# Optimization experiments

Measured on AMD Instinct MI355X. Metric: run time of the kernel, lower is better.

The kernel has to match this reference:

```python
import jax, jax.numpy as jnp
import numpy as np

B, S, D, H = 2, 2048, 1024, 16
DK = D // H


def setup_inputs() -> dict:
    key = jax.random.key(0)
    ks = jax.random.split(key, 12)
    scale = 1.0 / np.sqrt(D)
    inp = {
        "query": jax.random.normal(ks[0], (B, S, D), jnp.float32),
        "key": jax.random.normal(ks[1], (B, S, D), jnp.float32),
        "value": jax.random.normal(ks[2], (B, S, D), jnp.float32),
        "mask": jax.random.randint(ks[3], (B, 1, S, S), 0, 2, jnp.int32),
        "Wq": jax.random.normal(ks[4], (D, D), jnp.float32) * scale,
        "bq": jnp.zeros((D,), jnp.float32),
        "Wk": jax.random.normal(ks[5], (D, D), jnp.float32) * scale,
        "bk": jnp.zeros((D,), jnp.float32),
        "Wv": jax.random.normal(ks[6], (D, D), jnp.float32) * scale,
        "bv": jnp.zeros((D,), jnp.float32),
        "Wo": jax.random.normal(ks[7], (D, D), jnp.float32) * scale,
        "bo": jnp.zeros((D,), jnp.float32),
    }
    return inp


def reference(query, key, value, mask, Wq, bq, Wk, bk, Wv, bv, Wo, bo):
    # Linear projections (dropout is identity in eval mode)
    q = query @ Wq + bq          # (B,S,D)
    k = key @ Wk + bk
    v = value @ Wv + bv

    # split heads: (B,S,D) -> (B,H,S,DK)
    def split(x):
        return x.reshape(B, S, H, DK).transpose(0, 2, 1, 3)

    q, k, v = split(q), split(k), split(v)

    scores = jnp.einsum("bhqd,bhkd->bhqk", q, k) / jnp.sqrt(jnp.float32(DK))
    scores = jnp.where(mask == 0, jnp.float32(-1e9), scores)
    p_attn = jax.nn.softmax(scores, axis=-1)   # (B,H,S,S)

    att = jnp.einsum("bhqk,bhkd->bhqd", p_attn, v)  # (B,H,S,DK)
    merged = att.transpose(0, 2, 1, 3).reshape(B, S, D)
    return merged @ Wo + bo
```

## Files before the change

### kernel.cpp

```cpp
#include <hip/hip_runtime.h>
#include <hip/hip_bf16.h>
#include <cstdint>
#include <cstddef>


#define B_ 2
#define S_ 2048
#define D_ 1024
#define H_ 16
#define M_ 4096

typedef unsigned short u16;
typedef __attribute__((ext_vector_type(8))) short bf16x8;
typedef __attribute__((ext_vector_type(8))) unsigned short u16x8;
typedef __attribute__((ext_vector_type(4))) unsigned short u16x4;
typedef __attribute__((ext_vector_type(4))) unsigned int u32x4;
typedef __attribute__((ext_vector_type(4))) float f32x4;
typedef __attribute__((ext_vector_type(4))) int i32x4;

#define QSCALE 0.18033688011112042f

__device__ __forceinline__ u16 f2bf(float f) {
  __hip_bfloat16 h = __float2bfloat16(f);
  return *reinterpret_cast<u16*>(&h);
}

__device__ __forceinline__ unsigned cvtpk(float lo, float hi) {
  unsigned r;
  asm("v_cvt_pk_bf16_f32 %0, %1, %2" : "=v"(r) : "v"(lo), "v"(hi));
  return r;
}

__device__ __forceinline__ void gload_lds16(const void* g, void* l) {
  __builtin_amdgcn_global_load_lds((const __attribute__((address_space(1))) void*)g,
                                   (__attribute__((address_space(3))) void*)l, 16, 0, 0);
}

__global__ __launch_bounds__(256) void k_convert(const float* __restrict__ q, const float* __restrict__ k,
                                                 const float* __restrict__ v,
                                                 u16* __restrict__ xq, u16* __restrict__ xk, u16* __restrict__ xv) {
  int z = blockIdx.y;
  const float* src = (z == 0) ? q : (z == 1) ? k : v;
  u16* dst = (z == 0) ? xq : (z == 1) ? xk : xv;
  size_t i = ((size_t)blockIdx.x * 256 + threadIdx.x) * 8;
  f32x4 a = *(const f32x4*)(src + i);
  f32x4 b = *(const f32x4*)(src + i + 4);
  u16x8 o;
  o[0]=f2bf(a[0]); o[1]=f2bf(a[1]); o[2]=f2bf(a[2]); o[3]=f2bf(a[3]);
  o[4]=f2bf(b[0]); o[5]=f2bf(b[1]); o[6]=f2bf(b[2]); o[7]=f2bf(b[3]);
  *(u16x8*)(dst + i) = o;
}

__global__ __launch_bounds__(256) void k_transposeW(const float* __restrict__ w0, const float* __restrict__ w1,
                                                    const float* __restrict__ w2, const float* __restrict__ w3,
                                                    u16* __restrict__ t0, u16* __restrict__ t1,
                                                    u16* __restrict__ t2, u16* __restrict__ t3) {
  int z = blockIdx.z;
  const float* W = (z==0)?w0:(z==1)?w1:(z==2)?w2:w3;
  u16* Wt = (z==0)?t0:(z==1)?t1:(z==2)?t2:t3;
  __shared__ float tile[32][33];
  int tx = threadIdx.x & 31, ty = threadIdx.x >> 5;
  int bx = blockIdx.x * 32, by = blockIdx.y * 32;
  #pragma unroll
  for (int p = 0; p < 4; ++p)
    tile[ty + p*8][tx] = W[(size_t)(by + ty + p*8) * D_ + bx + tx];
  __syncthreads();
  #pragma unroll
  for (int p = 0; p < 4; ++p)
    Wt[(size_t)(bx + ty + p*8) * D_ + by + tx] = f2bf(tile[tx][ty + p*8]);
}

__global__ __launch_bounds__(256) void k_packmask(const int* __restrict__ mask, u16* __restrict__ out) {
  size_t t = (size_t)blockIdx.x * 256 + threadIdx.x;
  const int* p = mask + t * 64;
  unsigned wds0 = 0, wds1 = 0, wds2 = 0, wds3 = 0;
  #pragma unroll
  for (int c = 0; c < 16; ++c) {
    i32x4 v = *(const i32x4*)(p + c*4);
    #pragma unroll
    for (int e = 0; e < 4; ++e) {
      const int k = c*4 + e;
      const int lcw = (k >> 3) & 3;
      const int ni = ((k >> 4) & 2) | ((k >> 2) & 1);
      const unsigned bit = 1u << (4*ni + (k & 3));
      if (v[e]) {
        if (lcw == 0) wds0 |= bit; else if (lcw == 1) wds1 |= bit;
        else if (lcw == 2) wds2 |= bit; else wds3 |= bit;
      }
    }
  }
  u16x4 w; w[0] = (u16)wds0; w[1] = (u16)wds1; w[2] = (u16)wds2; w[3] = (u16)wds3;
  *(u16x4*)(out + t*4) = w;
}

template<int CMODE, int MI, int NI>
__device__ __forceinline__ void gemm_core(const u16* __restrict__ A, const u16* __restrict__ Bt,
                                          const float* __restrict__ bias, void* __restrict__ Cv, float scale) {
  extern __shared__ u16 sm[];
  constexpr int ASZ = MI*32*64;
  u16* As = sm;
  u16* Bs = sm + ASZ;
  const int t = threadIdx.x;
  const int l = t & 63, w = t >> 6;
  const int wr = w >> 1, wc = w & 1;
  const int lr = l & 15, lc = l >> 4;
  const int bm = blockIdx.x, bn = blockIdx.y;
  f32x4 acc[MI][NI];
  #pragma unroll
  for (int i = 0; i < MI; ++i)
    #pragma unroll
    for (int j = 0; j < NI; ++j) { f32x4 z = {0.f,0.f,0.f,0.f}; acc[i][j] = z; }
  const int srow = t >> 3;
  const int blkx = (t & 7) ^ (srow & 7);
  const u16* ga = A  + (size_t)(bm*(MI*32) + srow)*1024 + blkx*8;
  const u16* gb = Bt + (size_t)(bn*(NI*32) + srow)*1024 + blkx*8;
  for (int kt = 0; kt < 16; ++kt) {
    const int ko = kt * 64;
    __syncthreads();
    #pragma unroll
    for (int i = 0; i < MI; ++i)
      gload_lds16(ga + (size_t)(i*32)*1024 + ko, &As[i*2048 + t*8]);
    #pragma unroll
    for (int i = 0; i < NI; ++i)
      gload_lds16(gb + (size_t)(i*32)*1024 + ko, &Bs[i*2048 + t*8]);
    __syncthreads();
    #pragma unroll
    for (int ks = 0; ks < 2; ++ks) {
      bf16x8 af[MI], bfr[NI];
      #pragma unroll
      for (int mi = 0; mi < MI; ++mi)
        af[mi]  = *(const bf16x8*)&As[(wr*(MI*16) + mi*16 + lr)*64 + (((ks*4 + lc) ^ (lr & 7))*8)];
      #pragma unroll
      for (int ni = 0; ni < NI; ++ni)
        bfr[ni] = *(const bf16x8*)&Bs[(wc*(NI*16) + ni*16 + lr)*64 + (((ks*4 + lc) ^ (lr & 7))*8)];
      #pragma unroll
      for (int mi = 0; mi < MI; ++mi)
        #pragma unroll
        for (int ni = 0; ni < NI; ++ni)
          acc[mi][ni] = __builtin_amdgcn_mfma_f32_16x16x32_bf16(af[mi], bfr[ni], acc[mi][ni], 0, 0, 0);
    }
  }
  #pragma unroll
  for (int ni = 0; ni < NI; ++ni) {
    int gcol = bn*(NI*32) + wc*(NI*16) + ni*16 + lr;
    float bv = bias[gcol];
    #pragma unroll
    for (int mi = 0; mi < MI; ++mi) {
      int grow = bm*(MI*32) + wr*(MI*16) + mi*16 + lc*4;
      if (CMODE == 2) {
        u16x4 pk;
        #pragma unroll
        for (int j = 0; j < 4; ++j) pk[j] = f2bf((acc[mi][ni][j] + bv) * scale);
        *(u16x4*)&((u16*)Cv)[(size_t)gcol * M_ + grow] = pk;
      } else {
        #pragma unroll
        for (int j = 0; j < 4; ++j) {
          float v = (acc[mi][ni][j] + bv) * scale;
          if (CMODE == 0) ((u16*)Cv)[(size_t)(grow + j) * 1024 + gcol] = f2bf(v);
          else            ((float*)Cv)[(size_t)(grow + j) * 1024 + gcol] = v;
        }
      }
    }
  }
}

__global__ __launch_bounds__(256, 4) void k_gemm_qkv(const u16* Xq, const u16* Xk, const u16* Xv,
                                                     const u16* Wqt, const u16* Wkt, const u16* Wvt,
                                                     const float* bq, const float* bk, const float* bv,
                                                     u16* Qo, u16* Ko, u16* Vt, float qscale) {
  int z = blockIdx.z;
  if (z == 0)      gemm_core<0,4,4>(Xq, Wqt, bq, Qo, qscale);
  else if (z == 1) gemm_core<0,4,4>(Xk, Wkt, bk, Ko, 1.f);
  else             gemm_core<2,4,4>(Xv, Wvt, bv, Vt, 1.f);
}

__global__ __launch_bounds__(256, 4) void k_gemm_out(const u16* Aatt, const u16* Wot, const float* bo, float* out) {
  gemm_core<1,4,2>(Aatt, Wot, bo, out, 1.f);
}

__global__ __launch_bounds__(512, 4) void k_attn(const u16* __restrict__ Q, const u16* __restrict__ Kb,
                                                 const u16* __restrict__ Vt,
                                                 const u16* __restrict__ mbw,
                                                 u16* __restrict__ attb) {
  __shared__ u16 Ks[3*4096];
  __shared__ u16 Vs[2*4096];
  const int t = threadIdx.x, l = t & 63, w = t >> 6;
  const int lr = l & 15, lc = l >> 4;
  const int id = blockIdx.x + (blockIdx.y << 4) + (blockIdx.z << 8);
  const int lg = (id & 7) * 64 + (id >> 3);
  const int qt = lg & 15, h = (lg >> 4) & 15, b = lg >> 8;
  const int r0 = t >> 3;
  const int c0 = (t & 7) ^ (r0 & 7);
  const int pr0 = (r0 & 32) | ((r0 & 12) << 1) | ((r0 & 16) >> 2) | (r0 & 3);
  const u16* kp0 = Kb + (size_t)(b*S_ + pr0)*D_ + h*64 + c0*8;
  const u16* vp0 = Vt + (size_t)(h*64 + r0)*M_ + b*S_ + c0*8;

  gload_lds16(Q + (size_t)(b*S_ + qt*128 + r0)*D_      + h*64 + c0*8, &Ks[t*8]);
  gload_lds16(Q + (size_t)(b*S_ + qt*128 + 64 + r0)*D_ + h*64 + c0*8, &Ks[4096 + t*8]);
  __syncthreads();
  const int qrow = w*16 + lr;
  const int sw0 = ((lc     ) ^ (lr & 7)) * 8;
  const int sw1 = ((4 + lc ) ^ (lr & 7)) * 8;
  const int qbuf = (qrow >> 6) * 4096, qrl = (qrow & 63) * 64;
  bf16x8 aq0 = *(const bf16x8*)&Ks[qbuf + qrl + sw0];
  bf16x8 aq1 = *(const bf16x8*)&Ks[qbuf + qrl + sw1];
  __syncthreads();
  gload_lds16(kp0,                  &Ks[t*8]);
  gload_lds16(vp0,                  &Vs[t*8]);
  gload_lds16(kp0 + (size_t)64*D_,  &Ks[4096 + t*8]);

  const short one_bf = (short)0x3F80;
  const bf16x8 onesf = {one_bf,one_bf,one_bf,one_bf,one_bf,one_bf,one_bf,one_bf};
  f32x4 ls = {0.f,0.f,0.f,0.f};
  f32x4 o[4];
  #pragma unroll
  for (int ni = 0; ni < 4; ++ni) { f32x4 z = {0.f,0.f,0.f,0.f}; o[ni] = z; }
  const u16* mkp = mbw + (size_t)(b*S_ + qt*128 + qrow)*128 + lc;
  const u16* vpA = vp0;
  const u16* kpA = kp0;

#define AITER(N, KC, VC, VN, KNN, KPRE, VPRE, WAITN) {                                 \
    asm volatile("s_waitcnt vmcnt(" #WAITN ")");                                       \
    __builtin_amdgcn_s_barrier();                                                      \
    __builtin_amdgcn_sched_barrier(0);                                                 \
    unsigned mw = mkp[(N)*4];                                                          \
    if (VPRE) gload_lds16(vpA + ((N)+1)*64,              &Vs[(VN)*4096 + t*8]);        \
    if (KPRE) gload_lds16(kpA + (size_t)((N)+2)*64*D_,   &Ks[(KNN)*4096 + t*8]);       \
    f32x4 s[4];                                                                        \
    _Pragma("unroll")                                                                  \
    for (int ni = 0; ni < 4; ++ni) { f32x4 z = {0.f,0.f,0.f,0.f}; s[ni] = z; }         \
    __builtin_amdgcn_s_setprio(1);                                                     \
    _Pragma("unroll")                                                                  \
    for (int ni = 0; ni < 4; ++ni) {                                                   \
      bf16x8 bk0 = *(const bf16x8*)&Ks[(KC)*4096 + (ni*16 + lr)*64 + sw0];             \
      bf16x8 bk1 = *(const bf16x8*)&Ks[(KC)*4096 + (ni*16 + lr)*64 + sw1];             \
      s[ni] = __builtin_amdgcn_mfma_f32_16x16x32_bf16(bk0, aq0, s[ni], 0, 0, 0);       \
      s[ni] = __builtin_amdgcn_mfma_f32_16x16x32_bf16(bk1, aq1, s[ni], 0, 0, 0);       \
    }                                                                                  \
    __builtin_amdgcn_s_setprio(0);                                                     \
    _Pragma("unroll")                                                                  \
    for (int ni = 0; ni < 4; ++ni)                                                     \
      _Pragma("unroll")                                                                \
      for (int j = 0; j < 4; ++j) {                                                    \
        float pv = __builtin_amdgcn_exp2f(s[ni][j]);                                   \
        int bmsk = ((int)(mw << (31 - (4*ni + j)))) >> 31;                             \
        union { float f; int i; } u; u.f = pv; u.i &= bmsk;                            \
        s[ni][j] = u.f;                                                                \
      }                                                                                \
    u32x4 pw0, pw1;                                                                    \
    pw0[0] = cvtpk(s[0][0], s[0][1]); pw0[1] = cvtpk(s[0][2], s[0][3]);                \
    pw0[2] = cvtpk(s[1][0], s[1][1]); pw0[3] = cvtpk(s[1][2], s[1][3]);                \
    pw1[0] = cvtpk(s[2][0], s[2][1]); pw1[1] = cvtpk(s[2][2], s[2][3]);                \
    pw1[2] = cvtpk(s[3][0], s[3][1]); pw1[3] = cvtpk(s[3][2], s[3][3]);                \
    bf16x8 pa0 = __builtin_bit_cast(bf16x8, pw0);                                      \
    bf16x8 pa1 = __builtin_bit_cast(bf16x8, pw1);                                      \
    __builtin_amdgcn_s_setprio(1);                                                     \
    ls = __builtin_amdgcn_mfma_f32_16x16x32_bf16(pa0, onesf, ls, 0, 0, 0);             \
    ls = __builtin_amdgcn_mfma_f32_16x16x32_bf16(pa1, onesf, ls, 0, 0, 0);             \
    _Pragma("unroll")                                                                  \
    for (int ni = 0; ni < 4; ++ni) {                                                   \
      bf16x8 bv0 = *(const bf16x8*)&Vs[(VC)*4096 + (ni*16 + lr)*64 + sw0];             \
      o[ni] = __builtin_amdgcn_mfma_f32_16x16x32_bf16(pa0, bv0, o[ni], 0, 0, 0);       \
    }                                                                                  \
    _Pragma("unroll")                                                                  \
    for (int ni = 0; ni < 4; ++ni) {                                                   \
      bf16x8 bv1 = *(const bf16x8*)&Vs[(VC)*4096 + (ni*16 + lr)*64 + sw1];             \
      o[ni] = __builtin_amdgcn_mfma_f32_16x16x32_bf16(pa1, bv1, o[ni], 0, 0, 0);       \
    }                                                                                  \
    __builtin_amdgcn_s_setprio(0);                                                     \
  }

  for (int it = 0; it < 5; ++it) {
    AITER(0, 0,0, 1,2, 1,1, 1);
    AITER(1, 1,1, 0,0, 1,1, 1);
    AITER(2, 2,0, 1,1, 1,1, 1);
    AITER(3, 0,1, 0,2, 1,1, 1);
    AITER(4, 1,0, 1,0, 1,1, 1);
    AITER(5, 2,1, 0,1, 1,1, 1);
    mkp += 24;
    vpA += 6*64;
    kpA += (size_t)6*64*D_;
  }
  AITER(0, 0,0, 1,0, 0,1, 1);
  AITER(1, 1,1, 0,0, 0,0, 0);
#undef AITER

  float rl[4];
  #pragma unroll
  for (int j = 0; j < 4; ++j) rl[j] = 1.f / ls[j];
  #pragma unroll
  for (int ni = 0; ni < 4; ++ni)
    #pragma unroll
    for (int j = 0; j < 4; ++j) {
      int orow = qt*128 + w*16 + lc*4 + j, dcol = ni*16 + lr;
      attb[(size_t)(b*S_ + orow)*D_ + h*64 + dcol] = f2bf(o[ni][j] * rl[j]);
    }
}

extern "C" void kernel_launch(void* const* d_in, const int* in_sizes, int n_in,
                              void* d_out, int out_size, void* d_ws, size_t ws_size,
                              hipStream_t stream) {
  (void)in_sizes; (void)n_in; (void)out_size; (void)ws_size;
  const float* query = (const float*)d_in[0];
  const float* key   = (const float*)d_in[1];
  const float* value = (const float*)d_in[2];
  const int*   mask  = (const int*)d_in[3];
  const float* Wq = (const float*)d_in[4];
  const float* bq = (const float*)d_in[5];
  const float* Wk = (const float*)d_in[6];
  const float* bk = (const float*)d_in[7];
  const float* Wv = (const float*)d_in[8];
  const float* bv = (const float*)d_in[9];
  const float* Wo = (const float*)d_in[10];
  const float* bo = (const float*)d_in[11];
  float* out = (float*)d_out;
  char* ws = (char*)d_ws;
  const size_t MB = 1024 * 1024;
  u16* Xq  = (u16*)(ws + 0*MB);
  u16* Xk  = (u16*)(ws + 8*MB);
  u16* Xv  = (u16*)(ws + 16*MB);
  u16* Wqt = (u16*)(ws + 24*MB);
  u16* Wkt = (u16*)(ws + 26*MB);
  u16* Wvt = (u16*)(ws + 28*MB);
  u16* Wot = (u16*)(ws + 30*MB);
  u16* Qb  = (u16*)(ws + 32*MB);
  u16* Kb  = (u16*)(ws + 40*MB);
  u16* Vtb = (u16*)(ws + 48*MB);
  u16* mbits = (u16*)(ws + 56*MB);
  u16* attb = (u16*)(ws + 0*MB);

  k_convert  <<<dim3(2048, 3),     256, 0,     stream>>>(query, key, value, Xq, Xk, Xv);
  k_transposeW<<<dim3(32, 32, 4),  256, 0,     stream>>>(Wq, Wk, Wv, Wo, Wqt, Wkt, Wvt, Wot);
  k_packmask <<<dim3(512),         256, 0,     stream>>>(mask, mbits);
  k_gemm_qkv <<<dim3(32, 8, 3),    256, 32768, stream>>>(Xq, Xk, Xv, Wqt, Wkt, Wvt, bq, bk, bv,
                                                         Qb, Kb, Vtb, QSCALE);
  k_attn     <<<dim3(16, 16, 2),   512, 0,     stream>>>(Qb, Kb, Vtb, mbits, attb);
  k_gemm_out <<<dim3(32, 16),      256, 24576, stream>>>(attb, Wot, bo, out);
}
```

Baseline: 131.4 us.

## Merge prep kernels into one launch and double-buffer attention K/V in pairs

The convert, weight-transpose and mask-pack kernels become one launch whose blocks branch on their index, removing two kernel launches and the gaps between them. The attention loop moves from a 3-slot K / 2-slot V ring with one barrier per 64-key tile to a two-phase scheme. Each phase prefetches two K and two V tiles into the other half of a 4-slot buffer and then processes two tiles after a single __syncthreads. This halves the barriers and deepens the prefetch, at the cost of more LDS per block (64 KB), which may reduce occupancy. The explicit vmcnt waits are replaced by __syncthreads.

```diff
diff --git a/kernel.cpp b/kernel.cpp
--- a/kernel.cpp
+++ b/kernel.cpp
@@ -36,61 +36,66 @@
                                    (__attribute__((address_space(3))) void*)l, 16, 0, 0);
 }
 
-__global__ __launch_bounds__(256) void k_convert(const float* __restrict__ q, const float* __restrict__ k,
-                                                 const float* __restrict__ v,
-                                                 u16* __restrict__ xq, u16* __restrict__ xk, u16* __restrict__ xv) {
-  int z = blockIdx.y;
-  const float* src = (z == 0) ? q : (z == 1) ? k : v;
-  u16* dst = (z == 0) ? xq : (z == 1) ? xk : xv;
-  size_t i = ((size_t)blockIdx.x * 256 + threadIdx.x) * 8;
-  f32x4 a = *(const f32x4*)(src + i);
-  f32x4 b = *(const f32x4*)(src + i + 4);
-  u16x8 o;
-  o[0]=f2bf(a[0]); o[1]=f2bf(a[1]); o[2]=f2bf(a[2]); o[3]=f2bf(a[3]);
-  o[4]=f2bf(b[0]); o[5]=f2bf(b[1]); o[6]=f2bf(b[2]); o[7]=f2bf(b[3]);
-  *(u16x8*)(dst + i) = o;
-}
-
-__global__ __launch_bounds__(256) void k_transposeW(const float* __restrict__ w0, const float* __restrict__ w1,
-                                                    const float* __restrict__ w2, const float* __restrict__ w3,
-                                                    u16* __restrict__ t0, u16* __restrict__ t1,
-                                                    u16* __restrict__ t2, u16* __restrict__ t3) {
-  int z = blockIdx.z;
-  const float* W = (z==0)?w0:(z==1)?w1:(z==2)?w2:w3;
-  u16* Wt = (z==0)?t0:(z==1)?t1:(z==2)?t2:t3;
+__global__ __launch_bounds__(256) void k_prep(const float* __restrict__ q, const float* __restrict__ k,
+                                              const float* __restrict__ v,
+                                              u16* __restrict__ xq, u16* __restrict__ xk, u16* __restrict__ xv,
+                                              const float* __restrict__ w0, const float* __restrict__ w1,
+                                              const float* __restrict__ w2, const float* __restrict__ w3,
+                                              u16* __restrict__ t0, u16* __restrict__ t1,
+                                              u16* __restrict__ t2, u16* __restrict__ t3,
+                                              const int* __restrict__ mask, u16* __restrict__ mout) {
   __shared__ float tile[32][33];
-  int tx = threadIdx.x & 31, ty = threadIdx.x >> 5;
-  int bx = blockIdx.x * 32, by = blockIdx.y * 32;
-  #pragma unroll
-  for (int p = 0; p < 4; ++p)
-    tile[ty + p*8][tx] = W[(size_t)(by + ty + p*8) * D_ + bx + tx];
-  __syncthreads();
-  #pragma unroll
-  for (int p = 0; p < 4; ++p)
-    Wt[(size_t)(bx + ty + p*8) * D_ + by + tx] = f2bf(tile[tx][ty + p*8]);
-}
-
-__global__ __launch_bounds__(256) void k_packmask(const int* __restrict__ mask, u16* __restrict__ out) {
-  size_t t = (size_t)blockIdx.x * 256 + threadIdx.x;
-  const int* p = mask + t * 64;
-  unsigned wds0 = 0, wds1 = 0, wds2 = 0, wds3 = 0;
-  #pragma unroll
-  for (int c = 0; c < 16; ++c) {
-    i32x4 v = *(const i32x4*)(p + c*4);
-    #pragma unroll
-    for (int e = 0; e < 4; ++e) {
-      const int k = c*4 + e;
-      const int lcw = (k >> 3) & 3;
-      const int ni = ((k >> 4) & 2) | ((k >> 2) & 1);
-      const unsigned bit = 1u << (4*ni + (k & 3));
-      if (v[e]) {
-        if (lcw == 0) wds0 |= bit; else if (lcw == 1) wds1 |= bit;
-        else if (lcw == 2) wds2 |= bit; else wds3 |= bit;
+  const int id = blockIdx.x;
+  const int tid = threadIdx.x;
+  if (id < 6144) {
+    const int z = id >> 11;
+    const int bx = id & 2047;
+    const float* src = (z == 0) ? q : (z == 1) ? k : v;
+    u16* dst = (z == 0) ? xq : (z == 1) ? xk : xv;
+    size_t i = ((size_t)bx * 256 + tid) * 8;
+    f32x4 a = *(const f32x4*)(src + i);
+    f32x4 b = *(const f32x4*)(src + i + 4);
+    u16x8 o;
+    o[0]=f2bf(a[0]); o[1]=f2bf(a[1]); o[2]=f2bf(a[2]); o[3]=f2bf(a[3]);
+    o[4]=f2bf(b[0]); o[5]=f2bf(b[1]); o[6]=f2bf(b[2]); o[7]=f2bf(b[3]);
+    *(u16x8*)(dst + i) = o;
+  } else if (id < 10240) {
+    const int id2 = id - 6144;
+    const int z = id2 >> 10;
+    const int rem = id2 & 1023;
+    const int bx0 = (rem & 31) * 32, by0 = (rem >> 5) * 32;
+    const float* W = (z==0)?w0:(z==1)?w1:(z==2)?w2:w3;
+    u16* Wt = (z==0)?t0:(z==1)?t1:(z==2)?t2:t3;
+    int tx = tid & 31, ty = tid >> 5;
+    #pragma unroll
+    for (int p = 0; p < 4; ++p)
+      tile[ty + p*8][tx] = W[(size_t)(by0 + ty + p*8) * D_ + bx0 + tx];
+    __syncthreads();
+    #pragma unroll
+    for (int p = 0; p < 4; ++p)
+      Wt[(size_t)(bx0 + ty + p*8) * D_ + by0 + tx] = f2bf(tile[tx][ty + p*8]);
+  } else {
+    size_t tt = (size_t)(id - 10240) * 256 + tid;
+    const int* p = mask + tt * 64;
+    unsigned wds0 = 0, wds1 = 0, wds2 = 0, wds3 = 0;
+    #pragma unroll
+    for (int c = 0; c < 16; ++c) {
+      i32x4 vv = *(const i32x4*)(p + c*4);
+      #pragma unroll
+      for (int e = 0; e < 4; ++e) {
+        const int kk = c*4 + e;
+        const int lcw = (kk >> 3) & 3;
+        const int ni = ((kk >> 4) & 2) | ((kk >> 2) & 1);
+        const unsigned bit = 1u << (4*ni + (kk & 3));
+        if (vv[e]) {
+          if (lcw == 0) wds0 |= bit; else if (lcw == 1) wds1 |= bit;
+          else if (lcw == 2) wds2 |= bit; else wds3 |= bit;
+        }
       }
     }
-  }
-  u16x4 w; w[0] = (u16)wds0; w[1] = (u16)wds1; w[2] = (u16)wds2; w[3] = (u16)wds3;
-  *(u16x4*)(out + t*4) = w;
+    u16x4 w; w[0] = (u16)wds0; w[1] = (u16)wds1; w[2] = (u16)wds2; w[3] = (u16)wds3;
+    *(u16x4*)(mout + tt*4) = w;
+  }
 }
 
 template<int CMODE, int MI, int NI>
@@ -182,8 +187,8 @@
                                                  const u16* __restrict__ Vt,
                                                  const u16* __restrict__ mbw,
                                                  u16* __restrict__ attb) {
-  __shared__ u16 Ks[3*4096];
-  __shared__ u16 Vs[2*4096];
+  __shared__ u16 Ks[4*4096];
+  __shared__ u16 Vs[4*4096];
   const int t = threadIdx.x, l = t & 63, w = t >> 6;
   const int lr = l & 15, lc = l >> 4;
   const int id = blockIdx.x + (blockIdx.y << 4) + (blockIdx.z << 8);
@@ -208,6 +213,7 @@
   gload_lds16(kp0,                  &Ks[t*8]);
   gload_lds16(vp0,                  &Vs[t*8]);
   gload_lds16(kp0 + (size_t)64*D_,  &Ks[4096 + t*8]);
+  gload_lds16(vp0 + 64,             &Vs[4096 + t*8]);
 
   const short one_bf = (short)0x3F80;
   const bf16x8 onesf = {one_bf,one_bf,one_bf,one_bf,one_bf,one_bf,one_bf,one_bf};
@@ -216,24 +222,19 @@
   #pragma unroll
   for (int ni = 0; ni < 4; ++ni) { f32x4 z = {0.f,0.f,0.f,0.f}; o[ni] = z; }
   const u16* mkp = mbw + (size_t)(b*S_ + qt*128 + qrow)*128 + lc;
-  const u16* vpA = vp0;
-  const u16* kpA = kp0;
-
-#define AITER(N, KC, VC, VN, KNN, KPRE, VPRE, WAITN) {                                 \
-    asm volatile("s_waitcnt vmcnt(" #WAITN ")");                                       \
-    __builtin_amdgcn_s_barrier();                                                      \
-    __builtin_amdgcn_sched_barrier(0);                                                 \
-    unsigned mw = mkp[(N)*4];                                                          \
-    if (VPRE) gload_lds16(vpA + ((N)+1)*64,              &Vs[(VN)*4096 + t*8]);        \
-    if (KPRE) gload_lds16(kpA + (size_t)((N)+2)*64*D_,   &Ks[(KNN)*4096 + t*8]);       \
+  const u16* kpp = kp0;
+  const u16* vpp = vp0;
+
+#define ATILE(MN, SL) {                                                                \
+    unsigned mw = mkp[(MN)*4];                                                         \
     f32x4 s[4];                                                                        \
     _Pragma("unroll")                                                                  \
     for (int ni = 0; ni < 4; ++ni) { f32x4 z = {0.f,0.f,0.f,0.f}; s[ni] = z; }         \
     __builtin_amdgcn_s_setprio(1);                                                     \
     _Pragma("unroll")                                                                  \
     for (int ni = 0; ni < 4; ++ni) {                                                   \
-      bf16x8 bk0 = *(const bf16x8*)&Ks[(KC)*4096 + (ni*16 + lr)*64 + sw0];             \
-      bf16x8 bk1 = *(const bf16x8*)&Ks[(KC)*4096 + (ni*16 + lr)*64 + sw1];             \
+      bf16x8 bk0 = *(const bf16x8*)&Ks[(SL)*4096 + (ni*16 + lr)*64 + sw0];             \
+      bf16x8 bk1 = *(const bf16x8*)&Ks[(SL)*4096 + (ni*16 + lr)*64 + sw1];             \
       s[ni] = __builtin_amdgcn_mfma_f32_16x16x32_bf16(bk0, aq0, s[ni], 0, 0, 0);       \
       s[ni] = __builtin_amdgcn_mfma_f32_16x16x32_bf16(bk1, aq1, s[ni], 0, 0, 0);       \
     }                                                                                  \
@@ -259,31 +260,38 @@
     ls = __builtin_amdgcn_mfma_f32_16x16x32_bf16(pa1, onesf, ls, 0, 0, 0);             \
     _Pragma("unroll")                                                                  \
     for (int ni = 0; ni < 4; ++ni) {                                                   \
-      bf16x8 bv0 = *(const bf16x8*)&Vs[(VC)*4096 + (ni*16 + lr)*64 + sw0];             \
+      bf16x8 bv0 = *(const bf16x8*)&Vs[(SL)*4096 + (ni*16 + lr)*64 + sw0];             \
       o[ni] = __builtin_amdgcn_mfma_f32_16x16x32_bf16(pa0, bv0, o[ni], 0, 0, 0);       \
     }                                                                                  \
     _Pragma("unroll")                                                                  \
     for (int ni = 0; ni < 4; ++ni) {                                                   \
-      bf16x8 bv1 = *(const bf16x8*)&Vs[(VC)*4096 + (ni*16 + lr)*64 + sw1];             \
+      bf16x8 bv1 = *(const bf16x8*)&Vs[(SL)*4096 + (ni*16 + lr)*64 + sw1];             \
       o[ni] = __builtin_amdgcn_mfma_f32_16x16x32_bf16(pa1, bv1, o[ni], 0, 0, 0);       \
     }                                                                                  \
     __builtin_amdgcn_s_setprio(0);                                                     \
   }
 
-  for (int it = 0; it < 5; ++it) {
-    AITER(0, 0,0, 1,2, 1,1, 1);
-    AITER(1, 1,1, 0,0, 1,1, 1);
-    AITER(2, 2,0, 1,1, 1,1, 1);
-    AITER(3, 0,1, 0,2, 1,1, 1);
-    AITER(4, 1,0, 1,0, 1,1, 1);
-    AITER(5, 2,1, 0,1, 1,1, 1);
-    mkp += 24;
-    vpA += 6*64;
-    kpA += (size_t)6*64*D_;
-  }
-  AITER(0, 0,0, 1,0, 0,1, 1);
-  AITER(1, 1,1, 0,0, 0,0, 0);
-#undef AITER
+#define APHASE(PC, PRE) {                                                              \
+    __syncthreads();                                                                   \
+    if (PRE) {                                                                         \
+      gload_lds16(kpp + (size_t)2*64*D_, &Ks[((1-(PC))*2    )*4096 + t*8]);            \
+      gload_lds16(vpp + 2*64,            &Vs[((1-(PC))*2    )*4096 + t*8]);            \
+      gload_lds16(kpp + (size_t)3*64*D_, &Ks[((1-(PC))*2 + 1)*4096 + t*8]);            \
+      gload_lds16(vpp + 3*64,            &Vs[((1-(PC))*2 + 1)*4096 + t*8]);            \
+    }                                                                                  \
+    ATILE(0, (PC)*2);                                                                  \
+    ATILE(1, (PC)*2 + 1);                                                              \
+    kpp += (size_t)2*64*D_; vpp += 2*64; mkp += 8;                                     \
+  }
+
+  for (int it = 0; it < 7; ++it) {
+    APHASE(0, 1)
+    APHASE(1, 1)
+  }
+  APHASE(0, 1)
+  APHASE(1, 0)
+#undef APHASE
+#undef ATILE
 
   float rl[4];
   #pragma unroll
@@ -329,9 +337,9 @@
   u16* mbits = (u16*)(ws + 56*MB);
   u16* attb = (u16*)(ws + 0*MB);
 
-  k_convert  <<<dim3(2048, 3),     256, 0,     stream>>>(query, key, value, Xq, Xk, Xv);
-  k_transposeW<<<dim3(32, 32, 4),  256, 0,     stream>>>(Wq, Wk, Wv, Wo, Wqt, Wkt, Wvt, Wot);
-  k_packmask <<<dim3(512),         256, 0,     stream>>>(mask, mbits);
+  k_prep     <<<dim3(10752),       256, 0,     stream>>>(query, key, value, Xq, Xk, Xv,
+                                                         Wq, Wk, Wv, Wo, Wqt, Wkt, Wvt, Wot,
+                                                         mask, mbits);
   k_gemm_qkv <<<dim3(32, 8, 3),    256, 32768, stream>>>(Xq, Xk, Xv, Wqt, Wkt, Wvt, bq, bk, bv,
                                                          Qb, Kb, Vtb, QSCALE);
   k_attn     <<<dim3(16, 16, 2),   512, 0,     stream>>>(Qb, Kb, Vtb, mbits, attb);
```

Result: no change. 133.3 us (+1.5%).
